# Kernel optimization log

Hardware: AMD Instinct MI355X
Metric: run time of the kernel (lower is better)

The kernel has to match this reference:

```python
import jax, jax.numpy as jnp
import numpy as np
from jax import lax

D_MODEL, D_INNER, D_CONV, DT_RANK, D_STATE = 1024, 2048, 4, 64, 16
B_SZ, L = 1, 2048
EPS = 1e-5


def setup_inputs() -> dict:
    key = jax.random.key(0)
    ks = jax.random.split(key, 10)
    s = 0.02
    return {
        "x": jax.random.normal(ks[0], (B_SZ, L, D_MODEL), dtype=jnp.float32),
        "W_in": jax.random.normal(ks[1], (2 * D_INNER, D_MODEL), dtype=jnp.float32) * s,
        "conv_w": jax.random.normal(ks[2], (D_INNER, D_CONV), dtype=jnp.float32) * 0.1,
        "conv_b": jnp.zeros((D_INNER,), dtype=jnp.float32),
        "W_xproj": jax.random.normal(ks[3], (DT_RANK + 2 * D_STATE, D_INNER), dtype=jnp.float32) * s,
        "W_dt": jax.random.normal(ks[4], (D_INNER, DT_RANK), dtype=jnp.float32) * s,
        "b_dt": jnp.zeros((D_INNER,), dtype=jnp.float32),
        "A_log": jnp.broadcast_to(jnp.log(jnp.arange(1, D_STATE + 1, dtype=jnp.float32)), (D_INNER, D_STATE)).copy(),
        "D": jnp.ones((D_INNER,), dtype=jnp.float32),
        "W_out": jax.random.normal(ks[5], (D_MODEL, D_INNER), dtype=jnp.float32) * s,
        "norm_w": jnp.ones((D_MODEL,), dtype=jnp.float32),
    }


def _mamba_block(xn, W_in, conv_w, conv_b, W_xproj, W_dt, b_dt, A_log, D, W_out):
    b, l, _ = xn.shape
    # in_proj -> split into x branch and gate (res) branch
    xz = jnp.einsum("bld,ed->ble", xn, W_in)  # (b, l, 2*d_inner)
    xc, res = jnp.split(xz, 2, axis=-1)
    # depthwise causal conv1d over time (padding=d_conv-1, trimmed to l)
    xp = jnp.pad(xc, ((0, 0), (D_CONV - 1, 0), (0, 0)))
    conv = conv_b
    acc = jnp.zeros_like(xc)
    for k in range(D_CONV):
        acc = acc + xp[:, k:k + l, :] * conv_w[:, k]
    xs = jax.nn.silu(acc + conv_b)  # (b, l, d_inner)
    # x_proj -> delta (low-rank), B, C
    dbc = jnp.einsum("bld,ed->ble", xs, W_xproj)
    dt, Bm, Cm = jnp.split(dbc, [DT_RANK, DT_RANK + D_STATE], axis=-1)
    delta = jax.nn.softplus(jnp.einsum("blr,dr->bld", dt, W_dt) + b_dt)  # (b,l,d_inner)
    A = -jnp.exp(A_log)  # (d_inner, d_state)
    # discretize
    deltaA = jnp.exp(jnp.einsum("bld,dn->bldn", delta, A))
    dBu = jnp.einsum("bld,bln,bld->bldn", delta, Bm, xs)
    # selective scan over time
    def step(h, inp):
        dA_t, dBu_t, C_t = inp
        h = dA_t * h + dBu_t                      # (b, d_inner, d_state)
        y_t = jnp.einsum("bdn,bn->bd", h, C_t)
        return h, y_t
    h0 = jnp.zeros((b, D_INNER, D_STATE), dtype=xs.dtype)
    _, ys = lax.scan(step, h0, (deltaA.transpose(1, 0, 2, 3), dBu.transpose(1, 0, 2, 3), Cm.transpose(1, 0, 2)))
    y = ys.transpose(1, 0, 2) + xs * D  # (b, l, d_inner)
    y = y * jax.nn.silu(res)            # gate
    return jnp.einsum("bld,ed->ble", y, W_out)


def reference(x, W_in, conv_w, conv_b, W_xproj, W_dt, b_dt, A_log, D, W_out, norm_w):
    # RMSNorm
    xn = x * jax.lax.rsqrt(jnp.mean(x * x, axis=-1, keepdims=True) + EPS) * norm_w
    # Mamba mixer + residual
    return _mamba_block(xn, W_in, conv_w, conv_b, W_xproj, W_dt, b_dt, A_log, D, W_out) + x
```

## Files before the change

### kernel.cpp

```cpp
#include <hip/hip_runtime.h>
#include <hip/hip_bf16.h>

#define D_MODEL 1024
#define D_INNER 2048
#define DT_RANK 64
#define D_STATE 16
#define LSEQ    2048
#define CHUNK   32
#define NCHUNK  (LSEQ / CHUNK)
#define DN      (D_INNER * D_STATE)
#define KSPL_O  4
#define KSPL_X  16

typedef __attribute__((ext_vector_type(8))) short  short8;
typedef __attribute__((ext_vector_type(4))) float  float4v;
typedef __hip_bfloat16 bf16;

static __device__ __forceinline__ float b2f(bf16 v) { return __bfloat162float(v); }
static __device__ __forceinline__ bf16  f2b(float v) { return __float2bfloat16(v); }

#define GLOAD_LDS16(g, l)                                                          \
    __builtin_amdgcn_global_load_lds((const __attribute__((address_space(1))) void*)(g), \
                                     (__attribute__((address_space(3))) void*)(l), 16, 0, 0)

#define N1 (2 * D_INNER * D_MODEL)
#define N2 (D_MODEL * D_INNER)
#define N3 (96 * D_INNER)
#define N4 (D_INNER * DT_RANK)
#define NCAST4 ((N1 + N2 + N3 + N4) / 4)
__global__ __launch_bounds__(256)
void prep_kernel(const float* __restrict__ x, const float* __restrict__ nw,
                 bf16* __restrict__ xn,
                 const float* __restrict__ w_in, const float* __restrict__ w_out,
                 const float* __restrict__ w_xp, const float* __restrict__ w_dt,
                 bf16* __restrict__ o_in, bf16* __restrict__ o_out,
                 bf16* __restrict__ o_xp, bf16* __restrict__ o_dt) {
    int t = threadIdx.x;
    if (blockIdx.x < LSEQ) {
        int l = blockIdx.x;
        float4v v = ((const float4v*)(x + (size_t)l * D_MODEL))[t];
        float ssq = v[0]*v[0] + v[1]*v[1] + v[2]*v[2] + v[3]*v[3];
        for (int o = 32; o > 0; o >>= 1) ssq += __shfl_down(ssq, o);
        __shared__ float part[4];
        int lane = t & 63, wid = t >> 6;
        if (lane == 0) part[wid] = ssq;
        __syncthreads();
        float tot = part[0] + part[1] + part[2] + part[3];
        float sc = rsqrtf(tot * (1.0f / D_MODEL) + 1e-5f);
        float4v nv = ((const float4v*)nw)[t];
        bf16* op = xn + (size_t)l * D_MODEL + t * 4;
        op[0] = f2b(v[0] * sc * nv[0]);
        op[1] = f2b(v[1] * sc * nv[1]);
        op[2] = f2b(v[2] * sc * nv[2]);
        op[3] = f2b(v[3] * sc * nv[3]);
        return;
    }
    int i4 = (blockIdx.x - LSEQ) * 256 + t;
    if (i4 >= NCAST4) return;
    const float* src; bf16* dst; int base;
    if (i4 < N1 / 4)                { src = w_in;  dst = o_in;  base = 0; }
    else if (i4 < (N1 + N2) / 4)    { src = w_out; dst = o_out; base = N1 / 4; }
    else if (i4 < (N1+N2+N3) / 4)   { src = w_xp;  dst = o_xp;  base = (N1+N2) / 4; }
    else                            { src = w_dt;  dst = o_dt;  base = (N1+N2+N3) / 4; }
    int j = i4 - base;
    float4v v = ((const float4v*)src)[j];
    bf16* o = dst + j * 4;
    o[0] = f2b(v[0]); o[1] = f2b(v[1]); o[2] = f2b(v[2]); o[3] = f2b(v[3]);
}

template <int MODE>
__global__ __launch_bounds__(512)
void gemm_fast(const bf16* __restrict__ Ab, const bf16* __restrict__ Bb,
               int M, int N, int K, int kLen,
               float* __restrict__ outF, bf16* __restrict__ outB,
               const float* __restrict__ bias) {
    __shared__ short As[2][128 * 64];
    __shared__ short Bs[2][128 * 64];
    const short* Ap = (const short*)Ab;
    const short* Bp = (const short*)Bb;

    int t = threadIdx.x;
    int lane = t & 63, wid = t >> 6;
    int mBase = blockIdx.y * 128, nBase = blockIdx.x * 128;
    int kBase = blockIdx.z * kLen;
    int wm = 32 * (wid >> 1), wn = 64 * (wid & 1);
    int lr = lane & 15, quad = lane >> 4;

    int srow = 16 * wid + (lane >> 3);
    int cg = (lane & 7) ^ (lane >> 3);
    const short* gA = Ap + (size_t)(mBase + srow) * K + cg * 8;
    const short* gB = Bp + (size_t)(nBase + srow) * K + cg * 8;

    float4v acc[2][4] = {};

    #pragma unroll
    for (int g = 0; g < 2; ++g) {
        GLOAD_LDS16(gA + (size_t)g * 8 * K + kBase, &As[0][(16 * wid + g * 8) * 64]);
        GLOAD_LDS16(gB + (size_t)g * 8 * K + kBase, &Bs[0][(16 * wid + g * 8) * 64]);
    }

    int p = 0;
    for (int kt = kBase; kt < kBase + kLen; kt += 64, p ^= 1) {
        __syncthreads();
        if (kt + 64 < kBase + kLen) {
            int kn = kt + 64, q = p ^ 1;
            #pragma unroll
            for (int g = 0; g < 2; ++g) {
                GLOAD_LDS16(gA + (size_t)g * 8 * K + kn, &As[q][(16 * wid + g * 8) * 64]);
                GLOAD_LDS16(gB + (size_t)g * 8 * K + kn, &Bs[q][(16 * wid + g * 8) * 64]);
            }
        }
        #pragma unroll
        for (int s = 0; s < 2; ++s) {
            short8 af[2], bfr[4];
            #pragma unroll
            for (int i = 0; i < 2; ++i) {
                int row = wm + i * 16 + lr;
                af[i] = *(const short8*)&As[p][row * 64 + (((s * 4 + quad) ^ (lr & 7)) * 8)];
            }
            #pragma unroll
            for (int j = 0; j < 4; ++j) {
                int row = wn + j * 16 + lr;
                bfr[j] = *(const short8*)&Bs[p][row * 64 + (((s * 4 + quad) ^ (lr & 7)) * 8)];
            }
            #pragma unroll
            for (int i = 0; i < 2; ++i)
                #pragma unroll
                for (int j = 0; j < 4; ++j)
                    acc[i][j] = __builtin_amdgcn_mfma_f32_16x16x32_bf16(af[i], bfr[j], acc[i][j], 0, 0, 0);
        }
    }

    #pragma unroll
    for (int i = 0; i < 2; ++i) {
        #pragma unroll
        for (int j = 0; j < 4; ++j) {
            #pragma unroll
            for (int r = 0; r < 4; ++r) {
                int gm = mBase + wm + i * 16 + quad * 4 + r;
                int gn = nBase + wn + j * 16 + lr;
                float v = acc[i][j][r];
                if (MODE == 0) {
                    outB[(size_t)gm * N + gn] = f2b(v);
                } else if (MODE == 2) {
                    v += bias[gn];
                    v = (v > 20.0f) ? v : log1pf(__expf(v));
                    outB[(size_t)gm * N + gn] = f2b(v);
                } else {
                    outF[((size_t)blockIdx.z * M + gm) * N + gn] = v;
                }
            }
        }
    }
}

__global__ __launch_bounds__(128)
void reduce_xproj(const float* __restrict__ part, float* __restrict__ dbc,
                  bf16* __restrict__ dtb) {
    int m = blockIdx.x, j = threadIdx.x;
    if (j >= 96) return;
    float v = 0.0f;
    #pragma unroll
    for (int z = 0; z < KSPL_X; ++z)
        v += part[((size_t)z * LSEQ + m) * 128 + j];
    dbc[(size_t)m * 96 + j] = v;
    if (j < DT_RANK) dtb[(size_t)m * DT_RANK + j] = f2b(v);
}

__global__ __launch_bounds__(256)
void reduce_out(const float* __restrict__ part, const float* __restrict__ x,
                float* __restrict__ out) {
    int i = blockIdx.x * 256 + threadIdx.x;
    const int MN4 = LSEQ * D_MODEL / 4;
    float4v a = ((const float4v*)part)[i];
    #pragma unroll
    for (int z = 1; z < KSPL_O; ++z) {
        float4v b = ((const float4v*)part)[(size_t)z * MN4 + i];
        a[0] += b[0]; a[1] += b[1]; a[2] += b[2]; a[3] += b[3];
    }
    float4v xv = ((const float4v*)x)[i];
    a[0] += xv[0]; a[1] += xv[1]; a[2] += xv[2]; a[3] += xv[3];
    ((float4v*)out)[i] = a;
}

__global__ void conv_kernel(const bf16* __restrict__ xz, const float* __restrict__ cw,
                            const float* __restrict__ cb, bf16* __restrict__ xsb) {
    int idx = blockIdx.x * 256 + threadIdx.x;
    int c = idx & (D_INNER - 1);
    int l0 = (idx >> 11) * 4;
    float w0 = cw[c * 4 + 0], w1 = cw[c * 4 + 1];
    float w2 = cw[c * 4 + 2], w3 = cw[c * 4 + 3];
    float b = cb[c];
    const bf16* col = xz + c;
    float v[7];
    #pragma unroll
    for (int j = 0; j < 7; ++j) {
        int l = l0 - 3 + j;
        v[j] = (l >= 0) ? b2f(col[(size_t)l * (2 * D_INNER)]) : 0.0f;
    }
    #pragma unroll
    for (int j = 0; j < 4; ++j) {
        float acc = b + v[j] * w0 + v[j + 1] * w1 + v[j + 2] * w2 + v[j + 3] * w3;
        float s = acc * (1.0f / (1.0f + __expf(-acc)));
        xsb[(size_t)(l0 + j) * D_INNER + c] = f2b(s);
    }
}

template <int PASS>
__global__ __launch_bounds__(256)
void scan2(const bf16* __restrict__ delta, const bf16* __restrict__ xsb,
           const float* __restrict__ dbc, const bf16* __restrict__ xz,
           const float* __restrict__ A_log, const float* __restrict__ Dw,
           const float* __restrict__ Hinit,
           float* __restrict__ P, float* __restrict__ S, bf16* __restrict__ yg) {
    __shared__ float bc[CHUNK][32];
    int t = threadIdx.x;
    int d = blockIdx.x * 256 + t;
    int c = blockIdx.y;
    int l0 = c * CHUNK;

    {
        int row = t >> 3, col = (t & 7) * 4;
        *(float4v*)&bc[row][col] = *(const float4v*)&dbc[(size_t)(l0 + row) * 96 + 64 + col];
    }
    __syncthreads();

    float A[16], h[16], pr[16];
    #pragma unroll
    for (int n = 0; n < 16; ++n) A[n] = -__expf(A_log[(size_t)d * 16 + n]);
    if (PASS == 0) {
        #pragma unroll
        for (int n = 0; n < 16; ++n) { h[n] = 0.0f; pr[n] = 1.0f; }
    } else {
        #pragma unroll
        for (int n = 0; n < 16; n += 4)
            *(float4v*)&h[n] = *(const float4v*)&Hinit[(size_t)c * DN + (size_t)d * 16 + n];
    }
    float Dd = (PASS == 1) ? Dw[d] : 0.0f;

    for (int i = 0; i < CHUNK; ++i) {
        int l = l0 + i;
        float dv = b2f(delta[(size_t)l * D_INNER + d]);
        float xv = b2f(xsb[(size_t)l * D_INNER + d]);
        float u = dv * xv;
        float Bv[16];
        #pragma unroll
        for (int n = 0; n < 16; n += 4) *(float4v*)&Bv[n] = *(const float4v*)&bc[i][n];
        #pragma unroll
        for (int n = 0; n < 16; ++n) {
            float a = __expf(dv * A[n]);
            h[n] = fmaf(a, h[n], Bv[n] * u);
            if (PASS == 0) pr[n] *= a;
        }
        if (PASS == 1) {
            float Cv[16];
            #pragma unroll
            for (int n = 0; n < 16; n += 4) *(float4v*)&Cv[n] = *(const float4v*)&bc[i][16 + n];
            float y = xv * Dd;
            #pragma unroll
            for (int n = 0; n < 16; ++n) y = fmaf(h[n], Cv[n], y);
            float r = b2f(xz[(size_t)l * (2 * D_INNER) + D_INNER + d]);
            float g = r * (1.0f / (1.0f + __expf(-r)));
            yg[(size_t)l * D_INNER + d] = f2b(y * g);
        }
    }
    if (PASS == 0) {
        #pragma unroll
        for (int n = 0; n < 16; n += 4) {
            *(float4v*)&P[(size_t)c * DN + (size_t)d * 16 + n] = *(float4v*)&pr[n];
            *(float4v*)&S[(size_t)c * DN + (size_t)d * 16 + n] = *(float4v*)&h[n];
        }
    }
}

__global__ __launch_bounds__(256)
void scan_mid(const float* __restrict__ P, const float* __restrict__ S,
              float* __restrict__ Hinit) {
    int idx = blockIdx.x * 256 + threadIdx.x;
    float h = 0.0f;
    for (int c0 = 0; c0 < NCHUNK; c0 += 8) {
        float p[8], s[8];
        #pragma unroll
        for (int j = 0; j < 8; ++j) {
            p[j] = P[(size_t)(c0 + j) * DN + idx];
            s[j] = S[(size_t)(c0 + j) * DN + idx];
        }
        #pragma unroll
        for (int j = 0; j < 8; ++j) {
            Hinit[(size_t)(c0 + j) * DN + idx] = h;
            h = fmaf(p[j], h, s[j]);
        }
    }
}

extern "C" void kernel_launch(void* const* d_in, const int* in_sizes, int n_in,
                              void* d_out, int out_size, void* d_ws, size_t ws_size,
                              hipStream_t stream) {
    const float* x       = (const float*)d_in[0];
    const float* W_in    = (const float*)d_in[1];
    const float* conv_w  = (const float*)d_in[2];
    const float* conv_b  = (const float*)d_in[3];
    const float* W_xproj = (const float*)d_in[4];
    const float* W_dt    = (const float*)d_in[5];
    const float* b_dt    = (const float*)d_in[6];
    const float* A_log   = (const float*)d_in[7];
    const float* Dw      = (const float*)d_in[8];
    const float* W_out   = (const float*)d_in[9];
    const float* norm_w  = (const float*)d_in[10];

    char* w = (char*)d_ws;
    bf16* W_in_b    = (bf16*)w; w += (size_t)2 * D_INNER * D_MODEL * 2;
    bf16* W_out_b   = (bf16*)w; w += (size_t)D_MODEL * D_INNER * 2;
    bf16* W_xproj_b = (bf16*)w; w += (size_t)128 * D_INNER * 2;
    bf16* W_dt_b    = (bf16*)w; w += (size_t)D_INNER * DT_RANK * 2;
    char* reuse0 = w;
    bf16* xn        = (bf16*)w; w += (size_t)LSEQ * D_MODEL * 2;
    bf16* xz        = (bf16*)w; w += (size_t)LSEQ * 2 * D_INNER * 2;
    bf16* xsb       = (bf16*)w; w += (size_t)LSEQ * D_INNER * 2;
    bf16* delta     = (bf16*)w; w += (size_t)LSEQ * D_INNER * 2;
    float* dbc      = (float*)w; w += (size_t)LSEQ * 96 * 4;
    bf16* dtb       = (bf16*)w; w += (size_t)LSEQ * DT_RANK * 2;
    bf16* yg        = (bf16*)w; w += (size_t)LSEQ * D_INNER * 2;
    float* Pbuf     = (float*)w; w += (size_t)NCHUNK * DN * 4;
    float* Sbuf     = (float*)w; w += (size_t)NCHUNK * DN * 4;
    float* Hinit    = (float*)w; w += (size_t)NCHUNK * DN * 4;
    float* xp_part  = (float*)w; w += (size_t)KSPL_X * LSEQ * 128 * 4;
    float* out_part = (float*)reuse0;

    prep_kernel<<<LSEQ + (NCAST4 + 255) / 256, 256, 0, stream>>>(
        x, norm_w, xn, W_in, W_out, W_xproj, W_dt, W_in_b, W_out_b, W_xproj_b, W_dt_b);

    gemm_fast<0><<<dim3(4096 / 128, 2048 / 128, 1), 512, 0, stream>>>(
        xn, W_in_b, 2048, 4096, 1024, 1024, nullptr, xz, nullptr);

    conv_kernel<<<(LSEQ / 4 * D_INNER) / 256, 256, 0, stream>>>(xz, conv_w, conv_b, xsb);

    gemm_fast<4><<<dim3(1, 2048 / 128, KSPL_X), 512, 0, stream>>>(
        xsb, W_xproj_b, 2048, 128, 2048, 2048 / KSPL_X, xp_part, nullptr, nullptr);
    reduce_xproj<<<LSEQ, 128, 0, stream>>>(xp_part, dbc, dtb);

    gemm_fast<2><<<dim3(2048 / 128, 2048 / 128, 1), 512, 0, stream>>>(
        dtb, W_dt_b, 2048, 2048, 64, 64, nullptr, delta, b_dt);

    dim3 sgrid(D_INNER / 256, NCHUNK);
    scan2<0><<<sgrid, 256, 0, stream>>>(delta, xsb, dbc, xz, A_log, Dw,
                                        nullptr, Pbuf, Sbuf, nullptr);
    scan_mid<<<DN / 256, 256, 0, stream>>>(Pbuf, Sbuf, Hinit);
    scan2<1><<<sgrid, 256, 0, stream>>>(delta, xsb, dbc, xz, A_log, Dw,
                                        Hinit, nullptr, nullptr, yg);

    gemm_fast<4><<<dim3(1024 / 128, 2048 / 128, KSPL_O), 512, 0, stream>>>(
        yg, W_out_b, 2048, 1024, 2048, 2048 / KSPL_O, out_part, nullptr, nullptr);
    reduce_out<<<LSEQ * D_MODEL / 4 / 256, 256, 0, stream>>>(out_part, x, (float*)d_out);
}
```

Measured before the change: 242.0 us.

## Fuse chunked scan passes into cooperative kernel, remap GEMM blocks per XCD, vectorize conv

The three scan kernels (chunk-local pass, cross-chunk prefix, output pass) become one cooperative launch that uses grid-wide syncs and keeps per-thread state between phases. The GEMM remaps block indices so that blocks landing on the same XCD share A and B tiles, aiming for better L2 reuse. The conv kernel now handles two channels per thread with 32-bit loads and stores. The risks are cooperative-launch residency limits (512 blocks of 256 threads must all be co-resident) and the cost of the grid syncs.

```diff
diff --git a/kernel.cpp b/kernel.cpp
--- a/kernel.cpp
+++ b/kernel.cpp
@@ -1,5 +1,8 @@
 #include <hip/hip_runtime.h>
 #include <hip/hip_bf16.h>
+#include <hip/hip_cooperative_groups.h>
+
+namespace cg = cooperative_groups;
 
 #define D_MODEL 1024
 #define D_INNER 2048
@@ -18,6 +21,12 @@
 
 static __device__ __forceinline__ float b2f(bf16 v) { return __bfloat162float(v); }
 static __device__ __forceinline__ bf16  f2b(float v) { return __float2bfloat16(v); }
+static __device__ __forceinline__ float us2f(unsigned short u) {
+    union { unsigned int i; float f; } cc; cc.i = ((unsigned int)u) << 16; return cc.f;
+}
+static __device__ __forceinline__ unsigned short f2us(float v) {
+    return __bfloat16_as_ushort(__float2bfloat16(v));
+}
 
 #define GLOAD_LDS16(g, l)                                                          \
     __builtin_amdgcn_global_load_lds((const __attribute__((address_space(1))) void*)(g), \
@@ -81,15 +90,33 @@
 
     int t = threadIdx.x;
     int lane = t & 63, wid = t >> 6;
-    int mBase = blockIdx.y * 128, nBase = blockIdx.x * 128;
-    int kBase = blockIdx.z * kLen;
+
+    int bx, by, bz;
+    if (MODE == 0) {
+        int id = blockIdx.y * gridDim.x + blockIdx.x;
+        int xcd = id & 7, slot = id >> 3;
+        bx = (xcd & 3) * 8 + (slot & 7);
+        by = (xcd >> 2) * 8 + (slot >> 3);
+        bz = 0;
+    } else if (MODE == 4) {
+        int id = (blockIdx.z * gridDim.y + blockIdx.y) * gridDim.x + blockIdx.x;
+        int xcd = id & 7, slot = id >> 3;
+        bx = slot % gridDim.x;
+        int byz = xcd * ((gridDim.y * gridDim.z) / 8) + slot / gridDim.x;
+        by = byz % gridDim.y;
+        bz = byz / gridDim.y;
+    } else {
+        bx = blockIdx.x; by = blockIdx.y; bz = blockIdx.z;
+    }
+    int mBase = by * 128, nBase = bx * 128;
+    int kBase = bz * kLen;
     int wm = 32 * (wid >> 1), wn = 64 * (wid & 1);
     int lr = lane & 15, quad = lane >> 4;
 
     int srow = 16 * wid + (lane >> 3);
-    int cg = (lane & 7) ^ (lane >> 3);
-    const short* gA = Ap + (size_t)(mBase + srow) * K + cg * 8;
-    const short* gB = Bp + (size_t)(nBase + srow) * K + cg * 8;
+    int cg2 = (lane & 7) ^ (lane >> 3);
+    const short* gA = Ap + (size_t)(mBase + srow) * K + cg2 * 8;
+    const short* gB = Bp + (size_t)(nBase + srow) * K + cg2 * 8;
 
     float4v acc[2][4] = {};
 
@@ -147,7 +174,7 @@
                     v = (v > 20.0f) ? v : log1pf(__expf(v));
                     outB[(size_t)gm * N + gn] = f2b(v);
                 } else {
-                    outF[((size_t)blockIdx.z * M + gm) * N + gn] = v;
+                    outF[((size_t)bz * M + gm) * N + gn] = v;
                 }
             }
         }
@@ -186,33 +213,40 @@
 __global__ void conv_kernel(const bf16* __restrict__ xz, const float* __restrict__ cw,
                             const float* __restrict__ cb, bf16* __restrict__ xsb) {
     int idx = blockIdx.x * 256 + threadIdx.x;
-    int c = idx & (D_INNER - 1);
-    int l0 = (idx >> 11) * 4;
-    float w0 = cw[c * 4 + 0], w1 = cw[c * 4 + 1];
-    float w2 = cw[c * 4 + 2], w3 = cw[c * 4 + 3];
-    float b = cb[c];
-    const bf16* col = xz + c;
-    float v[7];
+    int c = (idx & (D_INNER / 2 - 1)) * 2;
+    int l0 = (idx >> 10) * 4;
+    float4v wA = ((const float4v*)cw)[c];
+    float4v wB = ((const float4v*)cw)[c + 1];
+    float bA = cb[c], bB = cb[c + 1];
+    const unsigned int* col = (const unsigned int*)((const unsigned short*)xz + c);
+    float vA[7], vB[7];
     #pragma unroll
     for (int j = 0; j < 7; ++j) {
         int l = l0 - 3 + j;
-        v[j] = (l >= 0) ? b2f(col[(size_t)l * (2 * D_INNER)]) : 0.0f;
+        if (l >= 0) {
+            unsigned int u = col[(size_t)l * D_INNER];
+            vA[j] = us2f((unsigned short)(u & 0xffff));
+            vB[j] = us2f((unsigned short)(u >> 16));
+        } else { vA[j] = 0.0f; vB[j] = 0.0f; }
     }
     #pragma unroll
     for (int j = 0; j < 4; ++j) {
-        float acc = b + v[j] * w0 + v[j + 1] * w1 + v[j + 2] * w2 + v[j + 3] * w3;
-        float s = acc * (1.0f / (1.0f + __expf(-acc)));
-        xsb[(size_t)(l0 + j) * D_INNER + c] = f2b(s);
-    }
-}
-
-template <int PASS>
+        float aA = bA + vA[j]*wA[0] + vA[j+1]*wA[1] + vA[j+2]*wA[2] + vA[j+3]*wA[3];
+        float aB = bB + vB[j]*wB[0] + vB[j+1]*wB[1] + vB[j+2]*wB[2] + vB[j+3]*wB[3];
+        float sA = aA * (1.0f / (1.0f + __expf(-aA)));
+        float sB = aB * (1.0f / (1.0f + __expf(-aB)));
+        unsigned int o = (unsigned int)f2us(sA) | ((unsigned int)f2us(sB) << 16);
+        *(unsigned int*)((unsigned short*)xsb + (size_t)(l0 + j) * D_INNER + c) = o;
+    }
+}
+
 __global__ __launch_bounds__(256)
-void scan2(const bf16* __restrict__ delta, const bf16* __restrict__ xsb,
-           const float* __restrict__ dbc, const bf16* __restrict__ xz,
-           const float* __restrict__ A_log, const float* __restrict__ Dw,
-           const float* __restrict__ Hinit,
-           float* __restrict__ P, float* __restrict__ S, bf16* __restrict__ yg) {
+void scan_fused(const bf16* __restrict__ delta, const bf16* __restrict__ xsb,
+                const float* __restrict__ dbc, const bf16* __restrict__ xz,
+                const float* __restrict__ A_log, const float* __restrict__ Dw,
+                float* __restrict__ P, float* __restrict__ S,
+                float* __restrict__ Hinit, bf16* __restrict__ yg) {
+    cg::grid_group grid = cg::this_grid();
     __shared__ float bc[CHUNK][32];
     int t = threadIdx.x;
     int d = blockIdx.x * 256 + t;
@@ -228,68 +262,68 @@
     float A[16], h[16], pr[16];
     #pragma unroll
     for (int n = 0; n < 16; ++n) A[n] = -__expf(A_log[(size_t)d * 16 + n]);
-    if (PASS == 0) {
-        #pragma unroll
-        for (int n = 0; n < 16; ++n) { h[n] = 0.0f; pr[n] = 1.0f; }
-    } else {
-        #pragma unroll
-        for (int n = 0; n < 16; n += 4)
-            *(float4v*)&h[n] = *(const float4v*)&Hinit[(size_t)c * DN + (size_t)d * 16 + n];
-    }
-    float Dd = (PASS == 1) ? Dw[d] : 0.0f;
-
+
+    #pragma unroll
+    for (int n = 0; n < 16; ++n) { h[n] = 0.0f; pr[n] = 1.0f; }
     for (int i = 0; i < CHUNK; ++i) {
         int l = l0 + i;
         float dv = b2f(delta[(size_t)l * D_INNER + d]);
         float xv = b2f(xsb[(size_t)l * D_INNER + d]);
         float u = dv * xv;
-        float Bv[16];
-        #pragma unroll
-        for (int n = 0; n < 16; n += 4) *(float4v*)&Bv[n] = *(const float4v*)&bc[i][n];
         #pragma unroll
         for (int n = 0; n < 16; ++n) {
             float a = __expf(dv * A[n]);
-            h[n] = fmaf(a, h[n], Bv[n] * u);
-            if (PASS == 0) pr[n] *= a;
-        }
-        if (PASS == 1) {
-            float Cv[16];
-            #pragma unroll
-            for (int n = 0; n < 16; n += 4) *(float4v*)&Cv[n] = *(const float4v*)&bc[i][16 + n];
-            float y = xv * Dd;
-            #pragma unroll
-            for (int n = 0; n < 16; ++n) y = fmaf(h[n], Cv[n], y);
-            float r = b2f(xz[(size_t)l * (2 * D_INNER) + D_INNER + d]);
-            float g = r * (1.0f / (1.0f + __expf(-r)));
-            yg[(size_t)l * D_INNER + d] = f2b(y * g);
-        }
-    }
-    if (PASS == 0) {
+            h[n] = fmaf(a, h[n], bc[i][n] * u);
+            pr[n] *= a;
+        }
+    }
+    #pragma unroll
+    for (int n = 0; n < 16; n += 4) {
+        *(float4v*)&P[(size_t)c * DN + (size_t)d * 16 + n] = *(float4v*)&pr[n];
+        *(float4v*)&S[(size_t)c * DN + (size_t)d * 16 + n] = *(float4v*)&h[n];
+    }
+
+    grid.sync();
+
+    int gid = (blockIdx.y * gridDim.x + blockIdx.x) * 256 + t;
+    if (gid < DN) {
+        float hh = 0.0f;
+        for (int c0 = 0; c0 < NCHUNK; c0 += 8) {
+            float pp[8], ss[8];
+            #pragma unroll
+            for (int j = 0; j < 8; ++j) {
+                pp[j] = P[(size_t)(c0 + j) * DN + gid];
+                ss[j] = S[(size_t)(c0 + j) * DN + gid];
+            }
+            #pragma unroll
+            for (int j = 0; j < 8; ++j) {
+                Hinit[(size_t)(c0 + j) * DN + gid] = hh;
+                hh = fmaf(pp[j], hh, ss[j]);
+            }
+        }
+    }
+
+    grid.sync();
+
+    #pragma unroll
+    for (int n = 0; n < 16; n += 4)
+        *(float4v*)&h[n] = *(const float4v*)&Hinit[(size_t)c * DN + (size_t)d * 16 + n];
+    float Dd = Dw[d];
+    for (int i = 0; i < CHUNK; ++i) {
+        int l = l0 + i;
+        float dv = b2f(delta[(size_t)l * D_INNER + d]);
+        float xv = b2f(xsb[(size_t)l * D_INNER + d]);
+        float u = dv * xv;
+        float y = xv * Dd;
         #pragma unroll
-        for (int n = 0; n < 16; n += 4) {
-            *(float4v*)&P[(size_t)c * DN + (size_t)d * 16 + n] = *(float4v*)&pr[n];
-            *(float4v*)&S[(size_t)c * DN + (size_t)d * 16 + n] = *(float4v*)&h[n];
-        }
-    }
-}
-
-__global__ __launch_bounds__(256)
-void scan_mid(const float* __restrict__ P, const float* __restrict__ S,
-              float* __restrict__ Hinit) {
-    int idx = blockIdx.x * 256 + threadIdx.x;
-    float h = 0.0f;
-    for (int c0 = 0; c0 < NCHUNK; c0 += 8) {
-        float p[8], s[8];
-        #pragma unroll
-        for (int j = 0; j < 8; ++j) {
-            p[j] = P[(size_t)(c0 + j) * DN + idx];
-            s[j] = S[(size_t)(c0 + j) * DN + idx];
-        }
-        #pragma unroll
-        for (int j = 0; j < 8; ++j) {
-            Hinit[(size_t)(c0 + j) * DN + idx] = h;
-            h = fmaf(p[j], h, s[j]);
-        }
+        for (int n = 0; n < 16; ++n) {
+            float a = __expf(dv * A[n]);
+            h[n] = fmaf(a, h[n], bc[i][n] * u);
+            y = fmaf(h[n], bc[i][16 + n], y);
+        }
+        float r = b2f(xz[(size_t)l * (2 * D_INNER) + D_INNER + d]);
+        float g = r * (1.0f / (1.0f + __expf(-r)));
+        yg[(size_t)l * D_INNER + d] = f2b(y * g);
     }
 }
 
@@ -333,7 +367,7 @@
     gemm_fast<0><<<dim3(4096 / 128, 2048 / 128, 1), 512, 0, stream>>>(
         xn, W_in_b, 2048, 4096, 1024, 1024, nullptr, xz, nullptr);
 
-    conv_kernel<<<(LSEQ / 4 * D_INNER) / 256, 256, 0, stream>>>(xz, conv_w, conv_b, xsb);
+    conv_kernel<<<(LSEQ / 4) * (D_INNER / 2) / 256, 256, 0, stream>>>(xz, conv_w, conv_b, xsb);
 
     gemm_fast<4><<<dim3(1, 2048 / 128, KSPL_X), 512, 0, stream>>>(
         xsb, W_xproj_b, 2048, 128, 2048, 2048 / KSPL_X, xp_part, nullptr, nullptr);
@@ -342,12 +376,13 @@
     gemm_fast<2><<<dim3(2048 / 128, 2048 / 128, 1), 512, 0, stream>>>(
         dtb, W_dt_b, 2048, 2048, 64, 64, nullptr, delta, b_dt);
 
-    dim3 sgrid(D_INNER / 256, NCHUNK);
-    scan2<0><<<sgrid, 256, 0, stream>>>(delta, xsb, dbc, xz, A_log, Dw,
-                                        nullptr, Pbuf, Sbuf, nullptr);
-    scan_mid<<<DN / 256, 256, 0, stream>>>(Pbuf, Sbuf, Hinit);
-    scan2<1><<<sgrid, 256, 0, stream>>>(delta, xsb, dbc, xz, A_log, Dw,
-                                        Hinit, nullptr, nullptr, yg);
+    {
+        void* args[] = {(void*)&delta, (void*)&xsb, (void*)&dbc, (void*)&xz,
+                        (void*)&A_log, (void*)&Dw, (void*)&Pbuf, (void*)&Sbuf,
+                        (void*)&Hinit, (void*)&yg};
+        hipLaunchCooperativeKernel((void*)scan_fused, dim3(D_INNER / 256, NCHUNK),
+                                   dim3(256), args, 0, stream);
+    }
 
     gemm_fast<4><<<dim3(1024 / 128, 2048 / 128, KSPL_O), 512, 0, stream>>>(
         yg, W_out_b, 2048, 1024, 2048, 2048 / KSPL_O, out_part, nullptr, nullptr);
```

After: 400.5 us. +65.5%, slower.
